# Kernel tuning notes

Hardware: AMD Instinct MI355X
Metric: run time of the kernel (lower is better)

Reference implementation:

```python
import jax, jax.numpy as jnp
import numpy as np

NUM_NODES = 200000   # graph size
E = 128              # embedding_size
B = 256              # batch of target nodes
M = 8                # num_metapaths
L = 64               # walk length (number of (n1,n2,e) triples per metapath)
NUM_EDGE_TYPE = 8
H = 8                # num_heads (hardcoded in module)


def setup_inputs() -> dict:
    key = jax.random.key(0)
    ks = jax.random.split(key, 10)
    # walks: last dim = (n1, n2, edge_type)
    n12 = jax.random.randint(ks[0], (B, M, L, 2), 0, NUM_NODES)
    ety = jax.random.randint(ks[1], (B, M, L, 1), 0, NUM_EDGE_TYPE)
    node_mp_walks = jnp.concatenate([n12, ety], axis=-1)
    node_idx = jax.random.randint(ks[2], (B,), 0, NUM_NODES)
    mp_type_idx = jnp.arange(M)
    # fc1(onehot(n)) == node_table[n] + fc1_b  (node_table = fc1.weight.T)
    node_table = jax.random.normal(ks[3], (NUM_NODES, E), dtype=jnp.float32) * 0.1
    fc1_b = jnp.zeros((E,), dtype=jnp.float32)
    edge_table = jax.random.normal(ks[4], (NUM_EDGE_TYPE, E), dtype=jnp.float32) * 0.1
    # Indexed_LinearFC_List: one (E,E) linear per metapath
    W_mp = jax.random.normal(ks[5], (M, E, E), dtype=jnp.float32) * 0.05
    b_mp = jnp.zeros((M, E), dtype=jnp.float32)
    # MultiheadAttention params (embed_dim=E, num_heads=H, eval mode -> no dropout)
    Wqkv = jax.random.normal(ks[6], (3 * E, E), dtype=jnp.float32) * 0.05
    bqkv = jnp.zeros((3 * E,), dtype=jnp.float32)
    Wo = jax.random.normal(ks[7], (E, E), dtype=jnp.float32) * 0.05
    bo = jnp.zeros((E,), dtype=jnp.float32)
    return dict(node_idx=node_idx, mp_type_idx=mp_type_idx, node_mp_walks=node_mp_walks,
                node_table=node_table, fc1_b=fc1_b, edge_table=edge_table,
                W_mp=W_mp, b_mp=b_mp, Wqkv=Wqkv, bqkv=bqkv, Wo=Wo, bo=bo)


def reference(node_idx, mp_type_idx, node_mp_walks, node_table, fc1_b, edge_table,
              W_mp, b_mp, Wqkv, bqkv, Wo, bo):
    n1 = node_mp_walks[..., 0]          # [B,M,L]
    n2 = node_mp_walks[..., 1]
    e = node_mp_walks[..., 2]
    # gather node/edge embeddings (fc1 over one-hot == table row + bias)
    n1_vec = node_table[n1] + fc1_b     # [B,M,L,E]
    n2_vec = node_table[n2] + fc1_b     # [B,M,L,E]
    edge_vec = edge_table[e]            # [B,M,L,E]
    # elementwise fuse + mean over walk steps
    mp_agg_0 = jnp.mean(n1_vec * n2_vec * edge_vec, axis=2)        # [B,M,E]
    # per-metapath indexed linear
    Wsel = W_mp[mp_type_idx]            # [M,E,E]
    bsel = b_mp[mp_type_idx]            # [M,E]
    mp_agg_1 = jnp.einsum('bme,meo->bmo', mp_agg_0, Wsel) + bsel   # [B,M,E]
    # self-attention over metapaths (torch MHA, seq-first layout: [M,B,E])
    x = jnp.transpose(mp_agg_1, (1, 0, 2))                         # [M,B,E]
    qkv = x @ Wqkv.T + bqkv                                        # [M,B,3E]
    q, k, v = jnp.split(qkv, 3, axis=-1)
    hd = E // H
    q = q.reshape(M, B, H, hd)
    k = k.reshape(M, B, H, hd)
    v = v.reshape(M, B, H, hd)
    scores = jnp.einsum('mbhd,nbhd->bhmn', q, k) / jnp.sqrt(jnp.float32(hd))
    attn = jax.nn.softmax(scores, axis=-1)                         # [B,H,M,M]
    o = jnp.einsum('bhmn,nbhd->mbhd', attn, v).reshape(M, B, E)
    attn_output = o @ Wo.T + bo                                    # [M,B,E]
    return attn_output
```

## Files before the change

kernel.cpp:

```cpp
#include <hip/hip_runtime.h>

#define B 256
#define M 8
#define L 64
#define E 128
#define H 8
#define HD 16
#define NET 8
#define E3 384

__global__ __launch_bounds__(256) void k_transpose(
    const float* __restrict__ Wqkv, const float* __restrict__ Wo,
    float* __restrict__ WqkvT, float* __restrict__ WoT) {
  int idx = blockIdx.x * 256 + threadIdx.x;
  if (idx < E * E3) {
    int e = idx / E3;
    int o = idx - e * E3;
    WqkvT[idx] = Wqkv[o * E + e];
  } else {
    int j = idx - E * E3;
    int e = j >> 7, o = j & 127;
    WoT[j] = Wo[o * E + e];
  }
}

__global__ __launch_bounds__(1024) void k_fused(
    const int* __restrict__ walks, const float* __restrict__ node_table,
    const float* __restrict__ fc1_b, const float* __restrict__ edge_table,
    const int* __restrict__ mp_type_idx,
    const float* __restrict__ W_mp, const float* __restrict__ b_mp,
    const float* __restrict__ WqkvT, const float* __restrict__ bqkv,
    const float* __restrict__ WoT, const float* __restrict__ bo,
    float* __restrict__ out) {
  __shared__ int    s_idx[M][L][3];
  __shared__ float  s_et[NET * E];
  __shared__ float4 s_red[32][32];
  __shared__ float  s_x[M][E];
  __shared__ float  s_y[M][E];
  __shared__ float  s_qkv[M][E3 + 1];
  __shared__ float  s_sc[H][M][M];
  __shared__ float  s_o[M][E];
  __shared__ int    s_mp[M];

  int b = blockIdx.x;
  int t = threadIdx.x;
  int g = t >> 5, lane = t & 31;

  const int* wb = walks + b * (M * L * 3);
  for (int idx = t; idx < M * L * 3; idx += 1024) ((int*)s_idx)[idx] = wb[idx];
  s_et[t] = edge_table[t];
  if (t < M) s_mp[t] = mp_type_idx[t];
  __syncthreads();

  {
    const float4* nt4 = (const float4*)node_table;
    float4 fb = ((const float4*)fc1_b)[lane];
    int m = g >> 2, q = g & 3;
    float4 acc = make_float4(0.f, 0.f, 0.f, 0.f);
    #pragma unroll
    for (int bi = 0; bi < 2; ++bi) {
      int l0 = q * 16 + bi * 8;
      float4 a[8], c[8];
      #pragma unroll
      for (int i = 0; i < 8; ++i) {
        int n1 = s_idx[m][l0 + i][0];
        int n2 = s_idx[m][l0 + i][1];
        a[i] = nt4[n1 * 32 + lane];
        c[i] = nt4[n2 * 32 + lane];
      }
      #pragma unroll
      for (int i = 0; i < 8; ++i) {
        int et = s_idx[m][l0 + i][2];
        float4 ev = ((const float4*)(s_et + et * E))[lane];
        acc.x += (a[i].x + fb.x) * (c[i].x + fb.x) * ev.x;
        acc.y += (a[i].y + fb.y) * (c[i].y + fb.y) * ev.y;
        acc.z += (a[i].z + fb.z) * (c[i].z + fb.z) * ev.z;
        acc.w += (a[i].w + fb.w) * (c[i].w + fb.w) * ev.w;
      }
    }
    s_red[g][lane] = acc;
  }
  __syncthreads();
  if (t < 256) {
    int m = t >> 5, ln = t & 31;
    float4 s = s_red[m * 4][ln];
    #pragma unroll
    for (int q = 1; q < 4; ++q) {
      float4 v = s_red[m * 4 + q][ln];
      s.x += v.x; s.y += v.y; s.z += v.z; s.w += v.w;
    }
    const float inv = 1.0f / (float)L;
    s.x *= inv; s.y *= inv; s.z *= inv; s.w *= inv;
    ((float4*)s_x[m])[ln] = s;
  }
  __syncthreads();

  {
    int m = t >> 7, o = t & 127;
    int mp = s_mp[m];
    const float* W = W_mp + mp * E * E;
    float acc = 0.f;
    for (int e = 0; e < E; ++e)
      acc += s_x[m][e] * W[e * E + o];
    s_y[m][o] = acc + b_mp[mp * E + o];
  }
  __syncthreads();

  if (t < 768) {
    int half = t / 384;
    int o = t - half * 384;
    float acc[4] = {0.f, 0.f, 0.f, 0.f};
    for (int e = 0; e < E; ++e) {
      float w = WqkvT[e * E3 + o];
      #pragma unroll
      for (int j = 0; j < 4; ++j) acc[j] += s_y[half * 4 + j][e] * w;
    }
    float bias = bqkv[o];
    #pragma unroll
    for (int j = 0; j < 4; ++j) s_qkv[half * 4 + j][o] = acc[j] + bias;
  }
  __syncthreads();

  if (t < 512) {
    int h = t >> 6, mq = (t >> 3) & 7, n = t & 7;
    float s = 0.f;
    #pragma unroll
    for (int d = 0; d < HD; ++d)
      s += s_qkv[mq][h * HD + d] * s_qkv[n][E + h * HD + d];
    s_sc[h][mq][n] = s * 0.25f;
  }
  __syncthreads();

  if (t < 64) {
    int h = t >> 3, mq = t & 7;
    float mx = -1e30f;
    #pragma unroll
    for (int n = 0; n < 8; ++n) mx = fmaxf(mx, s_sc[h][mq][n]);
    float ex[8];
    float sum = 0.f;
    #pragma unroll
    for (int n = 0; n < 8; ++n) { ex[n] = __expf(s_sc[h][mq][n] - mx); sum += ex[n]; }
    float inv = 1.0f / sum;
    #pragma unroll
    for (int n = 0; n < 8; ++n) s_sc[h][mq][n] = ex[n] * inv;
  }
  __syncthreads();

  {
    int mq = t >> 7, col = t & 127, h = col >> 4;
    float s = 0.f;
    #pragma unroll
    for (int n = 0; n < 8; ++n)
      s += s_sc[h][mq][n] * s_qkv[n][2 * E + col];
    s_o[mq][col] = s;
  }
  __syncthreads();

  if (t < 512) {
    int pm = t >> 7, o = t & 127;
    float acc[2] = {0.f, 0.f};
    for (int e = 0; e < E; ++e) {
      float w = WoT[e * E + o];
      acc[0] += s_o[pm * 2][e] * w;
      acc[1] += s_o[pm * 2 + 1][e] * w;
    }
    float bias = bo[o];
    out[((pm * 2) * B + b) * E + o]     = acc[0] + bias;
    out[((pm * 2 + 1) * B + b) * E + o] = acc[1] + bias;
  }
}

extern "C" void kernel_launch(void* const* d_in, const int* in_sizes, int n_in,
                              void* d_out, int out_size, void* d_ws, size_t ws_size,
                              hipStream_t stream) {
  const int*   mp_type_idx = (const int*)d_in[1];
  const int*   walks       = (const int*)d_in[2];
  const float* node_table  = (const float*)d_in[3];
  const float* fc1_b       = (const float*)d_in[4];
  const float* edge_table  = (const float*)d_in[5];
  const float* W_mp        = (const float*)d_in[6];
  const float* b_mp        = (const float*)d_in[7];
  const float* Wqkv        = (const float*)d_in[8];
  const float* bqkv        = (const float*)d_in[9];
  const float* Wo          = (const float*)d_in[10];
  const float* bo          = (const float*)d_in[11];
  float* out = (float*)d_out;

  char* ws = (char*)d_ws;
  float* WqkvT = (float*)(ws);
  float* WoT   = (float*)(ws + (256 << 10));

  k_transpose<<<dim3(256), dim3(256), 0, stream>>>(Wqkv, Wo, WqkvT, WoT);
  k_fused<<<dim3(B), dim3(1024), 0, stream>>>(
      walks, node_table, fc1_b, edge_table, mp_type_idx,
      W_mp, b_mp, WqkvT, bqkv, WoT, bo, out);
}
```

Baseline: 189.7 us.

## Split gather into per-(batch,metapath) kernel and fold weight transpose into it

The embedding gather and mean now run in a separate kernel with one 256-thread block per (batch, metapath) pair, 2048 blocks in total, so more work is spread across CUs and the latency-bound random loads are better hidden. The weight transpose is folded into this kernel, which removes the separate k_transpose launch. The attention stage becomes its own kernel that reads the aggregated vectors from workspace. In exchange there is an extra global round trip for agg0, and the WoT buffer moves to a new workspace offset.

```diff
diff --git a/kernel.cpp b/kernel.cpp
--- a/kernel.cpp
+++ b/kernel.cpp
@@ -9,90 +9,93 @@
 #define NET 8
 #define E3 384
 
-__global__ __launch_bounds__(256) void k_transpose(
-    const float* __restrict__ Wqkv, const float* __restrict__ Wo,
-    float* __restrict__ WqkvT, float* __restrict__ WoT) {
-  int idx = blockIdx.x * 256 + threadIdx.x;
-  if (idx < E * E3) {
-    int e = idx / E3;
-    int o = idx - e * E3;
-    WqkvT[idx] = Wqkv[o * E + e];
-  } else {
-    int j = idx - E * E3;
-    int e = j >> 7, o = j & 127;
-    WoT[j] = Wo[o * E + e];
-  }
-}
-
-__global__ __launch_bounds__(1024) void k_fused(
+__global__ __launch_bounds__(256, 4) void k_gather(
     const int* __restrict__ walks, const float* __restrict__ node_table,
     const float* __restrict__ fc1_b, const float* __restrict__ edge_table,
-    const int* __restrict__ mp_type_idx,
+    const float* __restrict__ Wqkv, const float* __restrict__ Wo,
+    float* __restrict__ WqkvT, float* __restrict__ WoT,
+    float* __restrict__ agg0) {
+  __shared__ int    s_idx[L][3];
+  __shared__ float  s_et[NET * E];
+  __shared__ float4 s_red[8][32];
+
+  int r = blockIdx.x;
+  int t = threadIdx.x;
+  int g = t >> 5, lane = t & 31;
+
+  if (t < L * 3) ((int*)s_idx)[t] = walks[r * (L * 3) + t];
+  #pragma unroll
+  for (int i = 0; i < 4; ++i) s_et[i * 256 + t] = edge_table[i * 256 + t];
+
+  if (t < 32) {
+    int el = r * 32 + t;
+    if (el < E * E3) {
+      int e = el / E3, o = el - e * E3;
+      WqkvT[el] = Wqkv[o * E + e];
+    } else {
+      int j = el - E * E3;
+      int e = j >> 7, o = j & 127;
+      WoT[j] = Wo[o * E + e];
+    }
+  }
+  __syncthreads();
+
+  const float4* nt4 = (const float4*)node_table;
+  float4 fb = ((const float4*)fc1_b)[lane];
+  float4 acc = make_float4(0.f, 0.f, 0.f, 0.f);
+  {
+    int l0 = g * 8;
+    float4 a[8], c[8];
+    #pragma unroll
+    for (int i = 0; i < 8; ++i) {
+      int n1 = s_idx[l0 + i][0];
+      int n2 = s_idx[l0 + i][1];
+      a[i] = nt4[n1 * 32 + lane];
+      c[i] = nt4[n2 * 32 + lane];
+    }
+    #pragma unroll
+    for (int i = 0; i < 8; ++i) {
+      int et = s_idx[l0 + i][2];
+      float4 ev = ((const float4*)(s_et + et * E))[lane];
+      acc.x += (a[i].x + fb.x) * (c[i].x + fb.x) * ev.x;
+      acc.y += (a[i].y + fb.y) * (c[i].y + fb.y) * ev.y;
+      acc.z += (a[i].z + fb.z) * (c[i].z + fb.z) * ev.z;
+      acc.w += (a[i].w + fb.w) * (c[i].w + fb.w) * ev.w;
+    }
+  }
+  s_red[g][lane] = acc;
+  __syncthreads();
+  if (t < 32) {
+    float4 s = s_red[0][t];
+    #pragma unroll
+    for (int gg = 1; gg < 8; ++gg) {
+      float4 v = s_red[gg][t];
+      s.x += v.x; s.y += v.y; s.z += v.z; s.w += v.w;
+    }
+    const float inv = 1.0f / (float)L;
+    s.x *= inv; s.y *= inv; s.z *= inv; s.w *= inv;
+    ((float4*)agg0)[r * 32 + t] = s;
+  }
+}
+
+__global__ __launch_bounds__(1024) void k_attn(
+    const float* __restrict__ agg0, const int* __restrict__ mp_type_idx,
     const float* __restrict__ W_mp, const float* __restrict__ b_mp,
     const float* __restrict__ WqkvT, const float* __restrict__ bqkv,
     const float* __restrict__ WoT, const float* __restrict__ bo,
     float* __restrict__ out) {
-  __shared__ int    s_idx[M][L][3];
-  __shared__ float  s_et[NET * E];
-  __shared__ float4 s_red[32][32];
-  __shared__ float  s_x[M][E];
-  __shared__ float  s_y[M][E];
-  __shared__ float  s_qkv[M][E3 + 1];
-  __shared__ float  s_sc[H][M][M];
-  __shared__ float  s_o[M][E];
-  __shared__ int    s_mp[M];
+  __shared__ float s_x[M][E];
+  __shared__ float s_y[M][E];
+  __shared__ float s_qkv[M][E3 + 1];
+  __shared__ float s_sc[H][M][M];
+  __shared__ float s_o[M][E];
+  __shared__ int   s_mp[M];
 
   int b = blockIdx.x;
   int t = threadIdx.x;
-  int g = t >> 5, lane = t & 31;
-
-  const int* wb = walks + b * (M * L * 3);
-  for (int idx = t; idx < M * L * 3; idx += 1024) ((int*)s_idx)[idx] = wb[idx];
-  s_et[t] = edge_table[t];
+
+  ((float*)s_x)[t] = agg0[b * (M * E) + t];
   if (t < M) s_mp[t] = mp_type_idx[t];
-  __syncthreads();
-
-  {
-    const float4* nt4 = (const float4*)node_table;
-    float4 fb = ((const float4*)fc1_b)[lane];
-    int m = g >> 2, q = g & 3;
-    float4 acc = make_float4(0.f, 0.f, 0.f, 0.f);
-    #pragma unroll
-    for (int bi = 0; bi < 2; ++bi) {
-      int l0 = q * 16 + bi * 8;
-      float4 a[8], c[8];
-      #pragma unroll
-      for (int i = 0; i < 8; ++i) {
-        int n1 = s_idx[m][l0 + i][0];
-        int n2 = s_idx[m][l0 + i][1];
-        a[i] = nt4[n1 * 32 + lane];
-        c[i] = nt4[n2 * 32 + lane];
-      }
-      #pragma unroll
-      for (int i = 0; i < 8; ++i) {
-        int et = s_idx[m][l0 + i][2];
-        float4 ev = ((const float4*)(s_et + et * E))[lane];
-        acc.x += (a[i].x + fb.x) * (c[i].x + fb.x) * ev.x;
-        acc.y += (a[i].y + fb.y) * (c[i].y + fb.y) * ev.y;
-        acc.z += (a[i].z + fb.z) * (c[i].z + fb.z) * ev.z;
-        acc.w += (a[i].w + fb.w) * (c[i].w + fb.w) * ev.w;
-      }
-    }
-    s_red[g][lane] = acc;
-  }
-  __syncthreads();
-  if (t < 256) {
-    int m = t >> 5, ln = t & 31;
-    float4 s = s_red[m * 4][ln];
-    #pragma unroll
-    for (int q = 1; q < 4; ++q) {
-      float4 v = s_red[m * 4 + q][ln];
-      s.x += v.x; s.y += v.y; s.z += v.z; s.w += v.w;
-    }
-    const float inv = 1.0f / (float)L;
-    s.x *= inv; s.y *= inv; s.z *= inv; s.w *= inv;
-    ((float4*)s_x[m])[ln] = s;
-  }
   __syncthreads();
 
   {
@@ -188,10 +191,11 @@
 
   char* ws = (char*)d_ws;
   float* WqkvT = (float*)(ws);
-  float* WoT   = (float*)(ws + (256 << 10));
-
-  k_transpose<<<dim3(256), dim3(256), 0, stream>>>(Wqkv, Wo, WqkvT, WoT);
-  k_fused<<<dim3(B), dim3(1024), 0, stream>>>(
-      walks, node_table, fc1_b, edge_table, mp_type_idx,
-      W_mp, b_mp, WqkvT, bqkv, WoT, bo, out);
+  float* WoT   = (float*)(ws + (192 << 10));
+  float* agg0  = (float*)(ws + (256 << 10));
+
+  k_gather<<<dim3(B * M), dim3(256), 0, stream>>>(
+      walks, node_table, fc1_b, edge_table, Wqkv, Wo, WqkvT, WoT, agg0);
+  k_attn<<<dim3(B), dim3(1024), 0, stream>>>(
+      agg0, mp_type_idx, W_mp, b_mp, WqkvT, bqkv, WoT, bo, out);
 }
```

After: 193.7 us. +2.1%, slower.
